# Kernel tuning notes

Hardware: AMD Instinct MI355X
Metric: run time of the kernel (lower is better)

The kernel has to match this reference:

```python
import jax, jax.numpy as jnp
import numpy as np

N_NODES = 50000
N_EDGES = 800000
IN_DIM = 128
EMB = 128
EDGE_DIM = 16
N_LAYERS = 4
BATCH = 64


def setup_inputs() -> dict:
    key = jax.random.key(0)
    ks = jax.random.split(key, 12)
    x = jax.random.normal(ks[0], (N_NODES, IN_DIM), dtype=jnp.float32)
    edge_index = jax.random.randint(ks[1], (2, N_EDGES), 0, N_NODES, dtype=jnp.int64)
    edge_attr = jax.random.normal(ks[2], (N_EDGES, EDGE_DIM), dtype=jnp.float32)
    batch = jnp.sort(jax.random.randint(ks[3], (N_NODES,), 0, BATCH, dtype=jnp.int64))

    def glorot(k, shape):
        fan_in = shape[-2]
        return jax.random.normal(k, shape, dtype=jnp.float32) / jnp.sqrt(jnp.float32(fan_in))

    msg_in = 2 * EMB + EDGE_DIM  # [h_src, h_dst, edge_attr]
    upd_in = 2 * EMB             # [h, aggregated_messages]
    return {
        "x": x,
        "edge_index": edge_index,
        "edge_attr": edge_attr,
        "batch": batch,
        "W_in": glorot(ks[4], (IN_DIM, EMB)),
        "b_in": jnp.zeros((EMB,), jnp.float32),
        "W_msg": glorot(ks[5], (N_LAYERS, msg_in, EMB)),
        "b_msg": jnp.zeros((N_LAYERS, EMB), jnp.float32),
        "W_upd": glorot(ks[6], (N_LAYERS, upd_in, EMB)),
        "b_upd": jnp.zeros((N_LAYERS, EMB), jnp.float32),
        "W_pred": glorot(ks[7], (EMB, 1)),
        "b_pred": jnp.zeros((1,), jnp.float32),
    }


def reference(x, edge_index, edge_attr, batch,
              W_in, b_in, W_msg, b_msg, W_upd, b_upd, W_pred, b_pred):
    n_nodes = x.shape[0]
    src, dst = edge_index[0], edge_index[1]

    # lin_in
    h = x @ W_in + b_in  # [N, EMB]

    # stacked message-passing layers with residual adds
    for l in range(W_msg.shape[0]):  # small fixed layer loop
        # per-edge message: relu(Linear([h_src, h_dst, e]))
        m_in = jnp.concatenate([h[src], h[dst], edge_attr], axis=-1)  # [E, 2*EMB+ED]
        m = jax.nn.relu(m_in @ W_msg[l] + b_msg[l])                    # [E, EMB]
        # sum-aggregate messages at destination nodes
        agg = jax.ops.segment_sum(m, dst, num_segments=n_nodes)       # [N, EMB]
        # node update: relu(Linear([h, agg])); residual add (h = h + conv(h))
        u_in = jnp.concatenate([h, agg], axis=-1)                      # [N, 2*EMB]
        h = h + jax.nn.relu(u_in @ W_upd[l] + b_upd[l])

    # global mean pool over graphs in the batch
    counts = jax.ops.segment_sum(jnp.ones((n_nodes,), h.dtype), batch, num_segments=BATCH)
    h_graph = jax.ops.segment_sum(h, batch, num_segments=BATCH) / jnp.maximum(counts, 1.0)[:, None]

    # lin_pred + view(-1)
    out = h_graph @ W_pred + b_pred  # [BATCH, 1]
    return out.reshape(-1)
```

## Files before the change

kernel.cpp:

```cpp
#include <hip/hip_runtime.h>


#define THREADS 256

typedef __attribute__((ext_vector_type(8))) short short8v;
typedef __attribute__((ext_vector_type(4))) float f32x4;

__device__ inline unsigned short f2bf(float f)
{
    unsigned int u = __float_as_uint(f);
    return (unsigned short)((u + 0x7FFFu + ((u >> 16) & 1u)) >> 16);
}

__global__ __launch_bounds__(THREADS)
void wconv_all(const float* __restrict__ W_in, const float* __restrict__ W_msg,
               const float* __restrict__ W_upd, unsigned short* __restrict__ wbf)
{
    int b = blockIdx.x;
    int job, kb;
    if (b < 576) { job = b >> 6; kb = b & 63; }
    else         { int r = b - 576; job = 9 + (r >> 7); kb = r & 127; }

    const float* src;
    unsigned short* dst;
    int K;
    if (job == 0)      { src = W_in;                                  dst = wbf;                               K = 128; }
    else if (job <= 4) { int l = job - 1; src = W_msg + (size_t)l * 272 * 128;             dst = wbf + 16384 + l * 32768;           K = 128; }
    else if (job <= 8) { int l = job - 5; src = W_msg + (size_t)l * 272 * 128 + 128 * 128; dst = wbf + 16384 + l * 32768 + 16384;   K = 128; }
    else               { int l = job - 9; src = W_upd + (size_t)l * 256 * 128;             dst = wbf + 147456 + l * 32768;          K = 256; }

    int i = kb * 256 + threadIdx.x;
    int k = i >> 7, n = i & 127;
    dst[n * K + k] = f2bf(src[i]);
}

__global__ __launch_bounds__(THREADS)
void f32_to_bf16(const float* __restrict__ in, unsigned short* __restrict__ out, int n4)
{
    int i = blockIdx.x * blockDim.x + threadIdx.x;
    int stride = gridDim.x * blockDim.x;
    for (; i < n4; i += stride) {
        float4 v = reinterpret_cast<const float4*>(in)[i];
        unsigned int lo = f2bf(v.x) | ((unsigned int)f2bf(v.y) << 16);
        unsigned int hi = f2bf(v.z) | ((unsigned int)f2bf(v.w) << 16);
        reinterpret_cast<uint2*>(out)[i] = make_uint2(lo, hi);
    }
}

template<int K, int CPW, bool FUSED2, bool RELU, bool RESID, bool WF32>
__global__ __launch_bounds__(THREADS)
void gemm_regW(const unsigned short* __restrict__ X1, const unsigned short* __restrict__ X2,
               const unsigned short* __restrict__ Wt, const float* __restrict__ bias,
               const float* __restrict__ resid, float* __restrict__ Cf,
               unsigned short* __restrict__ Cbf, unsigned short* __restrict__ Cbf2,
               int M, int nTiles)
{
    constexpr int KS = K / 32;
    const int t = threadIdx.x;
    const int w = t >> 6;
    const int l = t & 63;
    const int r  = l & 15;
    const int kb = l >> 4;
    const int wc = w * (CPW * 16);

    short8v b[CPW][KS];
#pragma unroll
    for (int c = 0; c < CPW; c++)
#pragma unroll
        for (int ks = 0; ks < KS; ks++)
            b[c][ks] = *reinterpret_cast<const short8v*>(
                Wt + (size_t)(wc + c * 16 + r) * K + ks * 32 + kb * 8);

    for (int tile = blockIdx.x; tile < nTiles; tile += gridDim.x) {
        const int mBase = tile * 32;
        const int row0 = min(mBase + r,      M - 1);
        const int row1 = min(mBase + 16 + r, M - 1);

        f32x4 acc[2][CPW];
#pragma unroll
        for (int mi = 0; mi < 2; mi++)
#pragma unroll
            for (int c = 0; c < CPW; c++) acc[mi][c] = (f32x4){0.f, 0.f, 0.f, 0.f};

#pragma unroll
        for (int ks = 0; ks < KS; ks++) {
            const unsigned short* Xs = X1;
            int ko = ks * 32;
            if (K == 256 && ko >= 128) { Xs = X2; ko -= 128; }
            const short8v a0 = *reinterpret_cast<const short8v*>(Xs + (size_t)row0 * 128 + ko + kb * 8);
            const short8v a1 = *reinterpret_cast<const short8v*>(Xs + (size_t)row1 * 128 + ko + kb * 8);
#pragma unroll
            for (int c = 0; c < CPW; c++) {
                acc[0][c] = __builtin_amdgcn_mfma_f32_16x16x32_bf16(a0, b[c][ks], acc[0][c], 0, 0, 0);
                acc[1][c] = __builtin_amdgcn_mfma_f32_16x16x32_bf16(a1, b[c][ks], acc[1][c], 0, 0, 0);
            }
        }

#pragma unroll
        for (int mi = 0; mi < 2; mi++) {
            const int rbase = mBase + mi * 16 + kb * 4;
#pragma unroll
            for (int c = 0; c < CPW; c++) {
                const int gc = wc + c * 16 + r;
#pragma unroll
                for (int j = 0; j < 4; j++) {
                    const int gr = rbase + j;
                    if (gr >= M) continue;
                    float v = acc[mi][c][j];
                    if (FUSED2) {
                        if (gc < 128) {
                            Cbf[(size_t)gr * 128 + gc] = f2bf(v);
                        } else {
                            v += bias[gc - 128];
                            Cbf2[(size_t)gr * 128 + gc - 128] = f2bf(v);
                        }
                    } else {
                        if (bias) v += bias[gc];
                        if (RELU)  v = fmaxf(v, 0.f);
                        if (RESID) v += resid[(size_t)gr * 128 + gc];
                        if (WF32)  Cf[(size_t)gr * 128 + gc] = v;
                        Cbf[(size_t)gr * 128 + gc] = f2bf(v);
                    }
                }
            }
        }
    }
}

__global__ __launch_bounds__(THREADS)
void zero_i32(int* __restrict__ p, int n)
{
    int i = blockIdx.x * blockDim.x + threadIdx.x;
    int stride = gridDim.x * blockDim.x;
    for (; i < n; i += stride) p[i] = 0;
}


__global__ __launch_bounds__(THREADS)
void csr_hist(const int* __restrict__ edst, int* __restrict__ deg, int nE)
{
    int i = blockIdx.x * blockDim.x + threadIdx.x;
    int stride = gridDim.x * blockDim.x;
    for (; i < nE; i += stride) atomicAdd(&deg[edst[i]], 1);
}

__global__ __launch_bounds__(THREADS)
void scan_stage1(const int* __restrict__ deg, int* __restrict__ incl,
                 int* __restrict__ psum, int n)
{
    __shared__ int buf[THREADS];
    const int t = threadIdx.x;
    const int base = blockIdx.x * 1024 + t * 4;

    int v0 = (base + 0 < n) ? deg[base + 0] : 0;
    int v1 = (base + 1 < n) ? deg[base + 1] : 0;
    int v2 = (base + 2 < n) ? deg[base + 2] : 0;
    int v3 = (base + 3 < n) ? deg[base + 3] : 0;
    const int s = v0 + v1 + v2 + v3;

    buf[t] = s;
    __syncthreads();
#pragma unroll
    for (int off = 1; off < THREADS; off <<= 1) {
        int x = (t >= off) ? buf[t - off] : 0;
        __syncthreads();
        buf[t] += x;
        __syncthreads();
    }
    const int excl = buf[t] - s;

    if (base + 0 < n) incl[base + 0] = excl + v0;
    if (base + 1 < n) incl[base + 1] = excl + v0 + v1;
    if (base + 2 < n) incl[base + 2] = excl + v0 + v1 + v2;
    if (base + 3 < n) incl[base + 3] = excl + s;
    if (t == THREADS - 1) psum[blockIdx.x] = buf[THREADS - 1];
}

__global__ __launch_bounds__(THREADS)
void scan_stage2(int* __restrict__ psum, int nb)
{
    __shared__ int buf[THREADS];
    const int t = threadIdx.x;
    int v = (t < nb) ? psum[t] : 0;
    buf[t] = v;
    __syncthreads();
#pragma unroll
    for (int off = 1; off < THREADS; off <<= 1) {
        int x = (t >= off) ? buf[t - off] : 0;
        __syncthreads();
        buf[t] += x;
        __syncthreads();
    }
    if (t < nb) psum[t] = buf[t] - v;
}

__global__ __launch_bounds__(THREADS)
void scan_stage3(const int* __restrict__ incl, const int* __restrict__ deg,
                 const int* __restrict__ psum, int* __restrict__ rowptr,
                 int* __restrict__ wp, int n, int nE)
{
    int i = blockIdx.x * blockDim.x + threadIdx.x;
    int stride = gridDim.x * blockDim.x;
    for (; i < n; i += stride) {
        int ex = incl[i] - deg[i] + psum[i >> 10];
        rowptr[i] = ex;
        wp[i]     = ex;
    }
    if (blockIdx.x == 0 && threadIdx.x == 0) rowptr[n] = nE;
}

__global__ __launch_bounds__(THREADS)
void csr_scatter(const int* __restrict__ esrc, const int* __restrict__ edst,
                 const float* __restrict__ eattr, int* __restrict__ wp,
                 int* __restrict__ col, float* __restrict__ eattrp, int nE)
{
    int i = blockIdx.x * blockDim.x + threadIdx.x;
    int stride = gridDim.x * blockDim.x;
    for (; i < nE; i += stride) {
        int d = edst[i];
        int pos = atomicAdd(&wp[d], 1);
        col[pos] = esrc[i];
        const float4* src4 = reinterpret_cast<const float4*>(eattr + (size_t)i * 16);
        float4*       dst4 = reinterpret_cast<float4*>(eattrp + (size_t)pos * 16);
        dst4[0] = src4[0]; dst4[1] = src4[1]; dst4[2] = src4[2]; dst4[3] = src4[3];
    }
}

__global__ __launch_bounds__(THREADS)
void edge_agg(const unsigned short* __restrict__ A, const unsigned short* __restrict__ Bb,
              const float* __restrict__ eattrp, const int* __restrict__ col,
              const int* __restrict__ rowptr, const float* __restrict__ Wm3,
              unsigned short* __restrict__ agg, int nN)
{
    __shared__ float W3s[16 * 128];
    const int t = threadIdx.x;

    *reinterpret_cast<float4*>(&W3s[t * 4])        = *reinterpret_cast<const float4*>(Wm3 + t * 4);
    *reinterpret_cast<float4*>(&W3s[1024 + t * 4]) = *reinterpret_cast<const float4*>(Wm3 + 1024 + t * 4);
    __syncthreads();

    const int lane = t & 63;
    const int wid  = __builtin_amdgcn_readfirstlane(t >> 6);
    const int d    = blockIdx.x * 4 + wid;
    if (d >= nN) return;

    float2 w[16];
#pragma unroll
    for (int k = 0; k < 16; k++)
        w[k] = *reinterpret_cast<const float2*>(&W3s[k * 128 + lane * 2]);

    const unsigned int bu = *reinterpret_cast<const unsigned int*>(Bb + (size_t)d * 128 + lane * 2);
    const float b0 = __uint_as_float(bu << 16);
    const float b1 = __uint_as_float(bu & 0xFFFF0000u);
    float2 acc = make_float2(0.f, 0.f);

    const int beg = rowptr[d], end = rowptr[d + 1];
    int e = beg;
    for (; e + 2 <= end; e += 2) {
        const int s0 = col[e];
        const int s1 = col[e + 1];
        const unsigned int au0 = *reinterpret_cast<const unsigned int*>(A + (size_t)s0 * 128 + lane * 2);
        const unsigned int au1 = *reinterpret_cast<const unsigned int*>(A + (size_t)s1 * 128 + lane * 2);
        const float4* p0 = reinterpret_cast<const float4*>(eattrp + (size_t)e * 16);
        const float4* p1 = reinterpret_cast<const float4*>(eattrp + (size_t)(e + 1) * 16);
        const float4 e00 = p0[0], e01 = p0[1], e02 = p0[2], e03 = p0[3];
        const float4 e10 = p1[0], e11 = p1[1], e12 = p1[2], e13 = p1[3];

        float v0x = __uint_as_float(au0 << 16) + b0;
        float v0y = __uint_as_float(au0 & 0xFFFF0000u) + b1;
        float v1x = __uint_as_float(au1 << 16) + b0;
        float v1y = __uint_as_float(au1 & 0xFFFF0000u) + b1;

        const float ek0[16] = {e00.x, e00.y, e00.z, e00.w, e01.x, e01.y, e01.z, e01.w,
                               e02.x, e02.y, e02.z, e02.w, e03.x, e03.y, e03.z, e03.w};
        const float ek1[16] = {e10.x, e10.y, e10.z, e10.w, e11.x, e11.y, e11.z, e11.w,
                               e12.x, e12.y, e12.z, e12.w, e13.x, e13.y, e13.z, e13.w};
#pragma unroll
        for (int k = 0; k < 16; k++) {
            v0x = fmaf(ek0[k], w[k].x, v0x);
            v0y = fmaf(ek0[k], w[k].y, v0y);
            v1x = fmaf(ek1[k], w[k].x, v1x);
            v1y = fmaf(ek1[k], w[k].y, v1y);
        }
        acc.x += fmaxf(v0x, 0.f) + fmaxf(v1x, 0.f);
        acc.y += fmaxf(v0y, 0.f) + fmaxf(v1y, 0.f);
    }
    if (e < end) {
        const int s = col[e];
        const unsigned int au = *reinterpret_cast<const unsigned int*>(A + (size_t)s * 128 + lane * 2);
        float vx = __uint_as_float(au << 16) + b0;
        float vy = __uint_as_float(au & 0xFFFF0000u) + b1;
        const float4* ea4 = reinterpret_cast<const float4*>(eattrp + (size_t)e * 16);
        const float4 f0 = ea4[0], f1 = ea4[1], f2 = ea4[2], f3 = ea4[3];
        const float ek[16] = {f0.x, f0.y, f0.z, f0.w, f1.x, f1.y, f1.z, f1.w,
                              f2.x, f2.y, f2.z, f2.w, f3.x, f3.y, f3.z, f3.w};
#pragma unroll
        for (int k = 0; k < 16; k++) {
            vx = fmaf(ek[k], w[k].x, vx);
            vy = fmaf(ek[k], w[k].y, vy);
        }
        acc.x += fmaxf(vx, 0.f);
        acc.y += fmaxf(vy, 0.f);
    }
    unsigned int o = (unsigned int)f2bf(acc.x) | ((unsigned int)f2bf(acc.y) << 16);
    *reinterpret_cast<unsigned int*>(agg + (size_t)d * 128 + lane * 2) = o;
}


__global__ __launch_bounds__(THREADS)
void pool_partial(const float* __restrict__ h, const int* __restrict__ batch,
                  float* __restrict__ hgsum, int n)
{
    const int t    = threadIdx.x;
    const int c    = t & 127;
    const int half = t >> 7;
    const int beg  = blockIdx.x * 256;
    const int end  = min(beg + 256, n);
    if (beg >= n) return;

    int   cur = -1;
    float acc = 0.f;
    for (int r = beg + half; r < end; r += 2) {
        int g = batch[r];
        if (g != cur) {
            if (cur >= 0) atomicAdd(&hgsum[(size_t)cur * 128 + c], acc);
            cur = g; acc = 0.f;
        }
        acc += h[(size_t)r * 128 + c];
    }
    if (cur >= 0) atomicAdd(&hgsum[(size_t)cur * 128 + c], acc);
}

__global__ __launch_bounds__(THREADS)
void pool_final(const float* __restrict__ hgsum, const int* __restrict__ batch,
                const float* __restrict__ Wp, const float* __restrict__ bp,
                float* __restrict__ out, int n)
{
    __shared__ float red[128];
    const int g = blockIdx.x;
    const int t = threadIdx.x;
    if (t >= 128) return;

    int lo, hi;
    {
        int a = 0, b = n;
        while (a < b) { int m = (a + b) >> 1; if (batch[m] < g) a = m + 1; else b = m; }
        lo = a;
        b = n;
        while (a < b) { int m = (a + b) >> 1; if (batch[m] < g + 1) a = m + 1; else b = m; }
        hi = a;
    }
    const int cnt = hi - lo;

    float v = hgsum[(size_t)g * 128 + t] / (float)max(cnt, 1);
    red[t] = v * Wp[t];
    __syncthreads();
    for (int off = 64; off > 0; off >>= 1) {
        if (t < off) red[t] += red[t + off];
        __syncthreads();
    }
    if (t == 0) out[g] = red[0] + bp[0];
}

extern "C" void kernel_launch(void* const* d_in, const int* in_sizes, int n_in,
                              void* d_out, int out_size, void* d_ws, size_t ws_size,
                              hipStream_t stream)
{
    const float* x      = (const float*)d_in[0];
    const int*   ei     = (const int*)  d_in[1];
    const float* eattr  = (const float*)d_in[2];
    const int*   batch  = (const int*)  d_in[3];
    const float* W_in   = (const float*)d_in[4];
    const float* b_in   = (const float*)d_in[5];
    const float* W_msg  = (const float*)d_in[6];
    const float* b_msg  = (const float*)d_in[7];
    const float* W_upd  = (const float*)d_in[8];
    const float* b_upd  = (const float*)d_in[9];
    const float* W_pred = (const float*)d_in[10];
    const float* b_pred = (const float*)d_in[11];
    float* out = (float*)d_out;

    const int nN = in_sizes[0] / 128;
    const int nE = in_sizes[1] / 2;
    const int* esrc = ei;
    const int* edst = ei + nE;

    float* h      = (float*)d_ws;
    float* eattrp = h + (size_t)nN * 128;
    float* hgsum  = eattrp + (size_t)nE * 16;
    unsigned short* xbf    = (unsigned short*)(hgsum + 8192);
    unsigned short* h_bf   = xbf    + (size_t)nN * 128;
    unsigned short* A_bf   = h_bf   + (size_t)nN * 128;
    unsigned short* Bb_bf  = A_bf   + (size_t)nN * 128;
    unsigned short* agg_bf = Bb_bf  + (size_t)nN * 128;
    unsigned short* wbf    = agg_bf + (size_t)nN * 128;
    unsigned short* wt_in  = wbf;
    unsigned short* wt_msg = wbf + 16384;
    unsigned short* wt_up  = wbf + 147456;
    int*   rowptr = (int*)(wbf + 278528);
    int*   wp     = rowptr + (nN + 1);
    int*   deg    = wp     + nN;
    int*   incl   = deg    + nN;
    int*   psum   = incl   + nN;
    int*   col    = psum   + 256;

    dim3 blk(THREADS);
    const int nTiles = (nN + 31) / 32;
    const int gGemm  = 1024;
    const int nChunks = (nN + 1023) / 1024;

    wconv_all<<<1088, blk, 0, stream>>>(W_in, W_msg, W_upd, wbf);
    f32_to_bf16<<<1024, blk, 0, stream>>>(x, xbf, nN * 128 / 4);

    zero_i32<<<64, blk, 0, stream>>>(deg, nN);
    csr_hist<<<256, blk, 0, stream>>>(edst, deg, nE);
    scan_stage1<<<nChunks, blk, 0, stream>>>(deg, incl, psum, nN);
    scan_stage2<<<1, blk, 0, stream>>>(psum, nChunks);
    scan_stage3<<<64, blk, 0, stream>>>(incl, deg, psum, rowptr, wp, nN, nE);
    csr_scatter<<<256, blk, 0, stream>>>(esrc, edst, eattr, wp, col, eattrp, nE);

    gemm_regW<128, 2, false, false, false, true><<<gGemm, blk, 0, stream>>>(
        xbf, nullptr, wt_in, b_in, nullptr, h, h_bf, nullptr, nN, nTiles);

    for (int l = 0; l < 4; l++) {
        const float* Wm3 = W_msg + (size_t)l * 272 * 128 + 256 * 128;
        const float* bm  = b_msg + l * 128;
        const float* bu  = b_upd + l * 128;

        gemm_regW<128, 4, true, false, false, false><<<gGemm, blk, 0, stream>>>(
            h_bf, nullptr, wt_msg + l * 32768, bm, nullptr, nullptr, A_bf, Bb_bf, nN, nTiles);

        edge_agg<<<(nN + 3) / 4, blk, 0, stream>>>(A_bf, Bb_bf, eattrp, col, rowptr, Wm3, agg_bf, nN);

        gemm_regW<256, 2, false, true, true, true><<<gGemm, blk, 0, stream>>>(
            h_bf, agg_bf, wt_up + l * 32768, bu, h, h, h_bf, nullptr, nN, nTiles);
    }

    zero_i32<<<16, blk, 0, stream>>>((int*)hgsum, 64 * 128);
    pool_partial<<<(nN + 255) / 256, blk, 0, stream>>>(h, batch, hgsum, nN);
    pool_final<<<64, blk, 0, stream>>>(hgsum, batch, W_pred, b_pred, out, nN);
}
```

Baseline: 687.7 us.

## Stage GEMM epilogue through LDS for vectorized stores and use packed FMA/bf16 convert

```diff
diff --git a/kernel.cpp b/kernel.cpp
--- a/kernel.cpp
+++ b/kernel.cpp
@@ -5,11 +5,19 @@
 
 typedef __attribute__((ext_vector_type(8))) short short8v;
 typedef __attribute__((ext_vector_type(4))) float f32x4;
+typedef __attribute__((ext_vector_type(2))) float f32x2;
 
 __device__ inline unsigned short f2bf(float f)
 {
     unsigned int u = __float_as_uint(f);
     return (unsigned short)((u + 0x7FFFu + ((u >> 16) & 1u)) >> 16);
+}
+
+__device__ inline unsigned int cvt_pk_bf16(float lo, float hi)
+{
+    unsigned int r;
+    asm("v_cvt_pk_bf16_f32 %0, %1, %2" : "=v"(r) : "v"(lo), "v"(hi));
+    return r;
 }
 
 __global__ __launch_bounds__(THREADS)
@@ -52,10 +60,14 @@
 void gemm_regW(const unsigned short* __restrict__ X1, const unsigned short* __restrict__ X2,
                const unsigned short* __restrict__ Wt, const float* __restrict__ bias,
                const float* __restrict__ resid, float* __restrict__ Cf,
-               unsigned short* __restrict__ Cbf, unsigned short* __restrict__ Cbf2,
+               unsigned short* __restrict__ CbfA, unsigned short* __restrict__ CbfB,
                int M, int nTiles)
 {
-    constexpr int KS = K / 32;
+    constexpr int KS  = K / 32;
+    constexpr int NC  = CPW * 64;
+    constexpr int LST = NC + 4;
+    __shared__ float Cls[32 * LST];
+
     const int t = threadIdx.x;
     const int w = t >> 6;
     const int l = t & 63;
@@ -71,6 +83,9 @@
             b[c][ks] = *reinterpret_cast<const short8v*>(
                 Wt + (size_t)(wc + c * 16 + r) * K + ks * 32 + kb * 8);
 
+    const int rrow = t >> 3;
+    const int cb   = (t & 7) * (NC / 8);
+
     for (int tile = blockIdx.x; tile < nTiles; tile += gridDim.x) {
         const int mBase = tile * 32;
         const int row0 = min(mBase + r,      M - 1);
@@ -97,33 +112,61 @@
         }
 
 #pragma unroll
-        for (int mi = 0; mi < 2; mi++) {
-            const int rbase = mBase + mi * 16 + kb * 4;
+        for (int mi = 0; mi < 2; mi++)
 #pragma unroll
             for (int c = 0; c < CPW; c++) {
                 const int gc = wc + c * 16 + r;
 #pragma unroll
-                for (int j = 0; j < 4; j++) {
-                    const int gr = rbase + j;
-                    if (gr >= M) continue;
-                    float v = acc[mi][c][j];
-                    if (FUSED2) {
-                        if (gc < 128) {
-                            Cbf[(size_t)gr * 128 + gc] = f2bf(v);
-                        } else {
-                            v += bias[gc - 128];
-                            Cbf2[(size_t)gr * 128 + gc - 128] = f2bf(v);
-                        }
-                    } else {
-                        if (bias) v += bias[gc];
-                        if (RELU)  v = fmaxf(v, 0.f);
-                        if (RESID) v += resid[(size_t)gr * 128 + gc];
-                        if (WF32)  Cf[(size_t)gr * 128 + gc] = v;
-                        Cbf[(size_t)gr * 128 + gc] = f2bf(v);
+                for (int j = 0; j < 4; j++)
+                    Cls[(mi * 16 + kb * 4 + j) * LST + gc] = acc[mi][c][j];
+            }
+        __syncthreads();
+
+        const int gr = mBase + rrow;
+        if (gr < M) {
+#pragma unroll
+            for (int q = 0; q < NC / 64; q += 1) {
+                f32x4 v0 = *reinterpret_cast<const f32x4*>(&Cls[rrow * LST + cb + q * 8]);
+                f32x4 v1 = *reinterpret_cast<const f32x4*>(&Cls[rrow * LST + cb + q * 8 + 4]);
+                const int col = cb + q * 8;
+
+                if (FUSED2) {
+                    if (col >= 128) {
+                        v0 += *reinterpret_cast<const f32x4*>(bias + col - 128);
+                        v1 += *reinterpret_cast<const f32x4*>(bias + col - 128 + 4);
                     }
+                } else if (bias) {
+                    v0 += *reinterpret_cast<const f32x4*>(bias + col);
+                    v1 += *reinterpret_cast<const f32x4*>(bias + col + 4);
+                }
+                if (RELU) {
+#pragma unroll
+                    for (int i = 0; i < 4; i++) { v0[i] = fmaxf(v0[i], 0.f); v1[i] = fmaxf(v1[i], 0.f); }
+                }
+                if (RESID) {
+                    v0 += *reinterpret_cast<const f32x4*>(resid + (size_t)gr * 128 + col);
+                    v1 += *reinterpret_cast<const f32x4*>(resid + (size_t)gr * 128 + col + 4);
+                }
+                if (WF32) {
+                    *reinterpret_cast<f32x4*>(Cf + (size_t)gr * 128 + col)     = v0;
+                    *reinterpret_cast<f32x4*>(Cf + (size_t)gr * 128 + col + 4) = v1;
+                }
+                uint4 pk;
+                pk.x = cvt_pk_bf16(v0[0], v0[1]);
+                pk.y = cvt_pk_bf16(v0[2], v0[3]);
+                pk.z = cvt_pk_bf16(v1[0], v1[1]);
+                pk.w = cvt_pk_bf16(v1[2], v1[3]);
+                if (FUSED2) {
+                    if (col < 128)
+                        *reinterpret_cast<uint4*>(CbfA + (size_t)gr * 128 + col) = pk;
+                    else
+                        *reinterpret_cast<uint4*>(CbfB + (size_t)gr * 128 + col - 128) = pk;
+                } else {
+                    *reinterpret_cast<uint4*>(CbfA + (size_t)gr * 128 + col) = pk;
                 }
             }
         }
+        __syncthreads();
     }
 }
 
@@ -244,15 +287,15 @@
     const int d    = blockIdx.x * 4 + wid;
     if (d >= nN) return;
 
-    float2 w[16];
+    f32x2 w[16];
 #pragma unroll
     for (int k = 0; k < 16; k++)
-        w[k] = *reinterpret_cast<const float2*>(&W3s[k * 128 + lane * 2]);
+        w[k] = *reinterpret_cast<const f32x2*>(&W3s[k * 128 + lane * 2]);
 
     const unsigned int bu = *reinterpret_cast<const unsigned int*>(Bb + (size_t)d * 128 + lane * 2);
-    const float b0 = __uint_as_float(bu << 16);
-    const float b1 = __uint_as_float(bu & 0xFFFF0000u);
-    float2 acc = make_float2(0.f, 0.f);
+    const f32x2 bv = (f32x2){__uint_as_float(bu << 16), __uint_as_float(bu & 0xFFFF0000u)};
+    const f32x2 zero = (f32x2){0.f, 0.f};
+    f32x2 acc = zero;
 
     const int beg = rowptr[d], end = rowptr[d + 1];
     int e = beg;
@@ -266,10 +309,8 @@
         const float4 e00 = p0[0], e01 = p0[1], e02 = p0[2], e03 = p0[3];
         const float4 e10 = p1[0], e11 = p1[1], e12 = p1[2], e13 = p1[3];
 
-        float v0x = __uint_as_float(au0 << 16) + b0;
-        float v0y = __uint_as_float(au0 & 0xFFFF0000u) + b1;
-        float v1x = __uint_as_float(au1 << 16) + b0;
-        float v1y = __uint_as_float(au1 & 0xFFFF0000u) + b1;
+        f32x2 v0 = (f32x2){__uint_as_float(au0 << 16), __uint_as_float(au0 & 0xFFFF0000u)} + bv;
+        f32x2 v1 = (f32x2){__uint_as_float(au1 << 16), __uint_as_float(au1 & 0xFFFF0000u)} + bv;
 
         const float ek0[16] = {e00.x, e00.y, e00.z, e00.w, e01.x, e01.y, e01.z, e01.w,
                                e02.x, e02.y, e02.z, e02.w, e03.x, e03.y, e03.z, e03.w};
@@ -277,33 +318,25 @@
                                e12.x, e12.y, e12.z, e12.w, e13.x, e13.y, e13.z, e13.w};
 #pragma unroll
         for (int k = 0; k < 16; k++) {
-            v0x = fmaf(ek0[k], w[k].x, v0x);
-            v0y = fmaf(ek0[k], w[k].y, v0y);
-            v1x = fmaf(ek1[k], w[k].x, v1x);
-            v1y = fmaf(ek1[k], w[k].y, v1y);
+            v0 = __builtin_elementwise_fma((f32x2){ek0[k], ek0[k]}, w[k], v0);
+            v1 = __builtin_elementwise_fma((f32x2){ek1[k], ek1[k]}, w[k], v1);
         }
-        acc.x += fmaxf(v0x, 0.f) + fmaxf(v1x, 0.f);
-        acc.y += fmaxf(v0y, 0.f) + fmaxf(v1y, 0.f);
+        acc += __builtin_elementwise_max(v0, zero) + __builtin_elementwise_max(v1, zero);
     }
     if (e < end) {
         const int s = col[e];
         const unsigned int au = *reinterpret_cast<const unsigned int*>(A + (size_t)s * 128 + lane * 2);
-        float vx = __uint_as_float(au << 16) + b0;
-        float vy = __uint_as_float(au & 0xFFFF0000u) + b1;
+        f32x2 v = (f32x2){__uint_as_float(au << 16), __uint_as_float(au & 0xFFFF0000u)} + bv;
         const float4* ea4 = reinterpret_cast<const float4*>(eattrp + (size_t)e * 16);
         const float4 f0 = ea4[0], f1 = ea4[1], f2 = ea4[2], f3 = ea4[3];
         const float ek[16] = {f0.x, f0.y, f0.z, f0.w, f1.x, f1.y, f1.z, f1.w,
                               f2.x, f2.y, f2.z, f2.w, f3.x, f3.y, f3.z, f3.w};
 #pragma unroll
-        for (int k = 0; k < 16; k++) {
-            vx = fmaf(ek[k], w[k].x, vx);
-            vy = fmaf(ek[k], w[k].y, vy);
-        }
-        acc.x += fmaxf(vx, 0.f);
-        acc.y += fmaxf(vy, 0.f);
-    }
-    unsigned int o = (unsigned int)f2bf(acc.x) | ((unsigned int)f2bf(acc.y) << 16);
-    *reinterpret_cast<unsigned int*>(agg + (size_t)d * 128 + lane * 2) = o;
+        for (int k = 0; k < 16; k++)
+            v = __builtin_elementwise_fma((f32x2){ek[k], ek[k]}, w[k], v);
+        acc += __builtin_elementwise_max(v, zero);
+    }
+    *reinterpret_cast<unsigned int*>(agg + (size_t)d * 128 + lane * 2) = cvt_pk_bf16(acc[0], acc[1]);
 }
 
 
```

Measured after the change: 651.7 us. 1.06x faster.
